# Kernel optimization log

Measured on AMD Instinct MI355X. Metric: run time of the kernel, lower is better.

Reference implementation:

```python
import jax, jax.numpy as jnp
import numpy as np

B, T, HID, H, Dk, Dv, K = 2, 1024, 1024, 8, 128, 128, 4
EPS = 1e-5


def _dwconv_causal(y, w, b):
    # y: [B,T,C], w: [C,1,K], b: [C]; torch Conv1d(padding=K-1) then [:, :, :T] == causal left-pad
    C = y.shape[-1]
    z = jnp.transpose(y, (0, 2, 1))  # [B,C,T]
    z = jax.lax.conv_general_dilated(
        z, w, window_strides=(1,), padding=[(K - 1, 0)],
        feature_group_count=C, dimension_numbers=("NCH", "OIH", "NCH"))
    z = z + b[None, :, None]
    return jnp.transpose(z, (0, 2, 1))


def _forward(x, Wq, Wk, Wv, conv_q_w, conv_q_b, conv_k_w, conv_k_b,
             conv_v_w, conv_v_b, Wa, ba, Wb, bb, Wg, Wo, ln_g, ln_b):
    b_, t_ = x.shape[0], x.shape[1]
    q = jax.nn.silu(_dwconv_causal(x @ Wq, conv_q_w, conv_q_b))
    k = jax.nn.silu(_dwconv_causal(x @ Wk, conv_k_w, conv_k_b))
    v = jax.nn.silu(_dwconv_causal(x @ Wv, conv_v_w, conv_v_b))
    q = q.reshape(b_, t_, H, Dk)
    k = k.reshape(b_, t_, H, Dk) * (Dk ** -0.5)
    v = v.reshape(b_, t_, H, Dv)
    alpha = jax.nn.sigmoid(x @ Wa + ba)  # [B,T,H]
    beta = jax.nn.sigmoid(x @ Wb + bb)   # [B,T,H]

    # time-major for scan
    qt = jnp.transpose(q, (1, 0, 2, 3))  # [T,B,H,Dk]
    kt = jnp.transpose(k, (1, 0, 2, 3))
    vt = jnp.transpose(v, (1, 0, 2, 3))  # [T,B,H,Dv]
    at = jnp.transpose(alpha, (1, 0, 2))  # [T,B,H]
    bt = jnp.transpose(beta, (1, 0, 2))

    def step(S, inp):
        q_t, k_t, v_t, a_t, b_t = inp
        sk = jnp.einsum('bhij,bhj->bhi', S, k_t)          # S @ k
        err = sk - v_t                                     # [B,H,Dv]
        S = a_t[:, :, None, None] * S - b_t[:, :, None, None] * (err[..., None] * k_t[:, :, None, :])
        o_t = jnp.einsum('bhij,bhj->bhi', S, q_t)          # S @ q (post-update)
        return S, o_t

    S0 = jnp.zeros((b_, H, Dv, Dk), x.dtype)
    _, o = jax.lax.scan(step, S0, (qt, kt, vt, at, bt))
    o = jnp.transpose(o, (1, 0, 2, 3))  # [B,T,H,Dv]

    # LayerNorm over Dv
    mu = jnp.mean(o, axis=-1, keepdims=True)
    var = jnp.mean((o - mu) ** 2, axis=-1, keepdims=True)
    o = (o - mu) * jax.lax.rsqrt(var + EPS) * ln_g + ln_b

    g = jax.nn.sigmoid(x @ Wg).reshape(b_, t_, H, Dv)
    o = (o * g).reshape(b_, t_, H * Dv)
    return o @ Wo


def setup_inputs() -> dict:
    key = jax.random.key(0)
    ks = jax.random.split(key, 18)
    s = 0.02

    def n(k, shape, scale=s):
        return jax.random.normal(k, shape, jnp.float32) * scale

    return {
        "x": jax.random.normal(ks[0], (B, T, HID), jnp.float32),
        "Wq": n(ks[1], (HID, H * Dk)),
        "Wk": n(ks[2], (HID, H * Dk)),
        "Wv": n(ks[3], (HID, H * Dv)),
        "conv_q_w": n(ks[4], (H * Dk, 1, K), 0.25),
        "conv_q_b": n(ks[5], (H * Dk,), 0.1),
        "conv_k_w": n(ks[6], (H * Dk, 1, K), 0.25),
        "conv_k_b": n(ks[7], (H * Dk,), 0.1),
        "conv_v_w": n(ks[8], (H * Dv, 1, K), 0.25),
        "conv_v_b": n(ks[9], (H * Dv,), 0.1),
        "Wa": n(ks[10], (HID, H)),
        "ba": n(ks[11], (H,), 0.1),
        "Wb": n(ks[12], (HID, H)),
        "bb": n(ks[13], (H,), 0.1),
        "Wg": n(ks[14], (HID, H * Dv)),
        "Wo": n(ks[15], (H * Dv, HID)),
        "ln_g": jnp.ones((Dv,), jnp.float32),
        "ln_b": jnp.zeros((Dv,), jnp.float32),
    }


def reference(x, Wq, Wk, Wv, conv_q_w, conv_q_b, conv_k_w, conv_k_b,
              conv_v_w, conv_v_b, Wa, ba, Wb, bb, Wg, Wo, ln_g, ln_b):
    return _forward(x, Wq, Wk, Wv, conv_q_w, conv_q_b, conv_k_w, conv_k_b,
                    conv_v_w, conv_v_b, Wa, ba, Wb, bb, Wg, Wo, ln_g, ln_b)
```

## Files before the change

kernel.cpp:

```cpp
#include <hip/hip_runtime.h>

#define TSEQ 1024
#define HID_ 1024
#define NH 8
#define DK 128
#define DV 128
#define ROWS 2048
#define SZf (ROWS * HID_)
#define LCH 64
#define NCK 16
#define KSTR 136
#define ESTR 65

typedef __attribute__((ext_vector_type(8))) short short8;
typedef __attribute__((ext_vector_type(4))) float f32x4;
#define MFMA __builtin_amdgcn_mfma_f32_16x16x32_bf16

__device__ __forceinline__ float sig_(float x) { return 1.f / (1.f + __expf(-x)); }

__device__ __forceinline__ ushort f2bf(float f) {
    unsigned int u = __builtin_bit_cast(unsigned int, f);
    u += 0x7FFF + ((u >> 16) & 1);
    return (ushort)(u >> 16);
}
__device__ __forceinline__ unsigned int pk2(float lo, float hi) {
    return (unsigned int)f2bf(lo) | ((unsigned int)f2bf(hi) << 16);
}

__global__ __launch_bounds__(256)
void k_x2bf(const float* __restrict__ x, ushort* __restrict__ xb)
{
    const size_t i8 = (size_t)blockIdx.x * 256 + threadIdx.x;
    float4 v0 = *(const float4*)(x + i8 * 8);
    float4 v1 = *(const float4*)(x + i8 * 8 + 4);
    uint4 o;
    o.x = pk2(v0.x, v0.y); o.y = pk2(v0.z, v0.w);
    o.z = pk2(v1.x, v1.y); o.w = pk2(v1.z, v1.w);
    *(uint4*)(xb + i8 * 8) = o;
}

__global__ __launch_bounds__(256)
void k_wT(const float* __restrict__ s0, const float* __restrict__ s1,
          const float* __restrict__ s2, const float* __restrict__ s3,
          ushort* __restrict__ dst)
{
    const int z = blockIdx.z;
    const float* W = (z == 0) ? s0 : (z == 1) ? s1 : (z == 2) ? s2 : s3;
    ushort* WT = dst + (size_t)z * (1024 * 1024);
    __shared__ float t[64][65];
    const int n0 = blockIdx.x * 64, k0 = blockIdx.y * 64;
    const int rr = threadIdx.x >> 4, cc = threadIdx.x & 15;
#pragma unroll
    for (int i = 0; i < 4; ++i) {
        const int row = i * 16 + rr;
        float4 v = *(const float4*)(W + (size_t)(k0 + row) * 1024 + n0 + cc * 4);
        t[row][cc * 4 + 0] = v.x; t[row][cc * 4 + 1] = v.y;
// ... 143 lines not shown
void k_conv_apply(float* __restrict__ q, float* __restrict__ k, float* __restrict__ v,
                  const float* __restrict__ scr,
                  const float* __restrict__ wq, const float* __restrict__ bq,
                  const float* __restrict__ wk, const float* __restrict__ bk,
                  const float* __restrict__ wv, const float* __restrict__ bv)
{
    const int z = blockIdx.z, b = blockIdx.y;
    const int j = blockIdx.x >> 2, cg = blockIdx.x & 3;
    float* y          = (z == 0) ? q  : (z == 1) ? k  : v;
    const float* w    = (z == 0) ? wq : (z == 1) ? wk : wv;
    const float* bias = (z == 0) ? bq : (z == 1) ? bk : bv;
    const float scale = (z == 1) ? 0.08838834764831845f : 1.f;
    const int c = cg * 256 + threadIdx.x;
    const float w0 = w[c * 4], w1 = w[c * 4 + 1], w2 = w[c * 4 + 2], w3 = w[c * 4 + 3];
    const float bs = bias[c];
    float y0 = 0.f, y1 = 0.f, y2 = 0.f;
    if (j > 0) {
        const float* s = scr + ((size_t)(z * 2 + b) * 15 + (j - 1)) * 3 * 1024 + c;
        y0 = s[0]; y1 = s[1024]; y2 = s[2048];
    }
    float* yp = y + ((size_t)b * TSEQ + j * 64) * HID_ + c;
#pragma unroll 4
    for (int t = 0; t < 64; ++t) {
        float y3  = yp[(size_t)t * HID_];
        float acc = fmaf(w0, y0, fmaf(w1, y1, fmaf(w2, y2, fmaf(w3, y3, bs))));
        float sv  = acc * sig_(acc) * scale;
        yp[(size_t)t * HID_] = sv;
        y0 = y1; y1 = y2; y2 = y3;
    }
}

__global__ __launch_bounds__(256)
void k_stage(const float* __restrict__ klin, const float* __restrict__ qlin,
             ushort* __restrict__ Kst, ushort* __restrict__ Qst,
             ushort* __restrict__ KTst)
{
    const int cid = blockIdx.x;
    const int bh = cid >> 4, c = cid & 15;
    const int b = bh >> 3, h = bh & 7;
    const int tid = threadIdx.x;
    const int t0 = c * LCH;
    __shared__ ushort Kl[64 * KSTR];
    const float* kb = klin + ((size_t)b * TSEQ + t0) * HID_ + h * DK;
    const float* qb = qlin + ((size_t)b * TSEQ + t0) * HID_ + h * DK;
    const size_t go = (size_t)cid * 8192;
#pragma unroll
    for (int j = 0; j < 8; ++j) {
        const int i4 = tid + j * 256;
        const int row = i4 >> 5, c4 = i4 & 31;
        float4 kv = *(const float4*)(kb + (size_t)row * HID_ + c4 * 4);
        float4 qv = *(const float4*)(qb + (size_t)row * HID_ + c4 * 4);
        uint2 kp; kp.x = pk2(kv.x, kv.y); kp.y = pk2(kv.z, kv.w);
        uint2 qp; qp.x = pk2(qv.x, qv.y); qp.y = pk2(qv.z, qv.w);
        *(uint2*)(Kst + go + row * 128 + c4 * 4) = kp;
        *(uint2*)(Qst + go + row * 128 + c4 * 4) = qp;
        *(uint2*)(Kl + row * KSTR + c4 * 4) = kp;
    }
    __syncthreads();
#pragma unroll
    for (int j = 0; j < 4; ++j) {
        const int o8 = tid + j * 256;
        const int dk = o8 >> 3, tt = (o8 & 7) * 8;
        ushort tmp[8];
#pragma unroll
        for (int e = 0; e < 8; ++e) tmp[e] = Kl[(tt + e) * KSTR + dk];
        *(uint4*)(KTst + go + dk * 64 + tt) = *(uint4*)tmp;
    }
}

__global__ __launch_bounds__(256)
void k_prep(const ushort* __restrict__ Kst, const ushort* __restrict__ Qst,
            const float* __restrict__ aT, const float* __restrict__ bT,
            ushort* __restrict__ Mg, ushort* __restrict__ Gg,
            float* __restrict__ pug, float* __restrict__ pog,
            float* __restrict__ cg, float* __restrict__ dtotg)
{
    const int cid = blockIdx.x;
    const int bh = cid >> 4, c = cid & 15;
    const int tid = threadIdx.x;
    const int t0 = c * LCH;

    __shared__ ushort Kb[64 * KSTR], Qb[64 * KSTR];
    __shared__ float Ef[64 * ESTR];
    __shared__ float Mf[64 * ESTR];
    __shared__ float cums[64], bv[64];

    if (tid < 64) {
        const float a = aT[(size_t)bh * TSEQ + t0 + tid];
        bv[tid] = bT[(size_t)bh * TSEQ + t0 + tid];
        float cs = __logf(a);
#pragma unroll
        for (int d = 1; d < 64; d <<= 1) {
            float pv = __shfl_up(cs, d);
            if (tid >= d) cs += pv;
        }
        cums[tid] = cs;
    }
    const size_t go = (size_t)cid * 8192;
#pragma unroll
// ... 41 lines not shown

    if (tid < 64) {
        const int s = tid;
        for (int r = 0; r < 64; ++r) Mf[r * ESTR + s] = 0.f;
        Mf[s * ESTR + s] = bv[s];
        for (int t = 1; t < 64; ++t) {
            float s0 = 0.f, s1 = 0.f;
            int r = 0;
            for (; r + 1 < t; r += 2) {
                s0 = fmaf(Ef[t * ESTR + r],     Mf[r * ESTR + s],       s0);
                s1 = fmaf(Ef[t * ESTR + r + 1], Mf[(r + 1) * ESTR + s], s1);
            }
            if (r < t) s0 = fmaf(Ef[t * ESTR + r], Mf[r * ESTR + s], s0);
            if (s < t) Mf[t * ESTR + s] = -bv[t] * (s0 + s1);
        }
    }
    __syncthreads();
    ushort* Mc = Mg + (size_t)cid * 4096;
#pragma unroll
    for (int j = 0; j < 16; ++j) {
        const int e = tid + j * 256;
        Mc[e] = f2bf(Mf[(e >> 6) * ESTR + (e & 63)]);
    }
    if (tid < 64) {
        const float cp = (tid > 0) ? cums[tid - 1] : 0.f;
        pug[cid * 64 + tid] = __expf(cp);
        pog[cid * 64 + tid] = __expf(cums[tid]);
        cg [cid * 64 + tid] = __expf(cums[63] - cums[tid]);
        if (tid == 0) dtotg[cid] = __expf(cums[63]);
    }
}

__global__ __launch_bounds__(256)
void k_scan2(const ushort* __restrict__ Kst, const ushort* __restrict__ Qst,
             const ushort* __restrict__ KTst, const float* __restrict__ vlin,
             const ushort* __restrict__ Mg, const ushort* __restrict__ Gg,
             const float* __restrict__ pug, const float* __restrict__ pog,
             const float* __restrict__ cg, const float* __restrict__ dtotg,
             float* __restrict__ o)
{
    const int blk = blockIdx.x;
    const int bh = blk >> 2, rb = blk & 3;
    const int b = bh >> 3, h = bh & 7;
    const int tid = threadIdx.x;
    const int wv = tid >> 6, l = tid & 63, l15 = l & 15, lq = l >> 4;
    const int k8o = lq * 8;

    __shared__ ushort Kb[64 * KSTR], Qb[64 * KSTR];
    __shared__ ushort KTb[128 * 72];
    __shared__ float  Vtf[32 * 72];
    __shared__ ushort Mb[64 * 72], Gb[64 * 72];
    __shared__ ushort Shb[32 * KSTR], Slb[32 * KSTR];
    __shared__ ushort Yb[32 * 72], Wb[32 * 72], Wcb[32 * 72];
    __shared__ float  Otf[64 * 36];
    __shared__ float  puv[64], pov[64], cv2[64], dts[1];

    const int trow  = wv >> 1;
    const int tcol0 = (wv & 1) * 2;
    const int scol0 = (wv & 1) * 4;

    f32x4 accS[4];
#pragma unroll
    for (int m = 0; m < 4; ++m) accS[m] = f32x4{0.f, 0.f, 0.f, 0.f};

    const float* vbase = vlin + (size_t)b * TSEQ * HID_ + h * DV + rb * 32;
    float* obase = o + (size_t)bh * TSEQ * DV + rb * 32;

    uint4 rk[4], rq[4], rkt[4], rm[2], rg[2];
    float4 rv[2];
    float rpu = 0.f, rpo = 0.f, rcv = 0.f, rdt = 0.f;

    auto LOADC = [&](int cc) {
        const int cid = bh * 16 + cc;
        const size_t go = (size_t)cid * 8192;
#pragma unroll
        for (int j = 0; j < 4; ++j) {
            rk[j]  = *(const uint4*)(Kst  + go + (tid + j * 256) * 8);
            rq[j]  = *(const uint4*)(Qst  + go + (tid + j * 256) * 8);
            rkt[j] = *(const uint4*)(KTst + go + (tid + j * 256) * 8);
        }
#pragma unroll
        for (int j = 0; j < 2; ++j) {
            rm[j] = *(const uint4*)(Mg + (size_t)cid * 4096 + (tid + j * 256) * 8);
            rg[j] = *(const uint4*)(Gg + (size_t)cid * 4096 + (tid + j * 256) * 8);
            const int i4 = tid + j * 256;
            rv[j] = *(const float4*)(vbase + (size_t)(cc * LCH + (i4 >> 3)) * HID_ + (i4 & 7) * 4);
        }
        if (tid < 64) {
            rpu = pug[cid * 64 + tid];
            rpo = pog[cid * 64 + tid];
            rcv = cg [cid * 64 + tid];
            if (tid == 0) rdt = dtotg[cid];
        }
    };
    auto WRITEC = [&]() {
#pragma unroll
        for (int j = 0; j < 4; ++j) {
            const int i16 = tid + j * 256;
            *(uint4*)(Kb  + (i16 >> 4) * KSTR + (i16 & 15) * 8) = rk[j];
            *(uint4*)(Qb  + (i16 >> 4) * KSTR + (i16 & 15) * 8) = rq[j];
            *(uint4*)(KTb + (i16 >> 3) * 72   + (i16 & 7) * 8)  = rkt[j];
        }
#pragma unroll
        for (int j = 0; j < 2; ++j) {
            const int i8 = tid + j * 256;
            *(uint4*)(Mb + (i8 >> 3) * 72 + (i8 & 7) * 8) = rm[j];
            *(uint4*)(Gb + (i8 >> 3) * 72 + (i8 & 7) * 8) = rg[j];
            const int i4 = tid + j * 256;
            const int row = i4 >> 3, c4 = i4 & 7;
            Vtf[(c4 * 4 + 0) * 72 + row] = rv[j].x;
            Vtf[(c4 * 4 + 1) * 72 + row] = rv[j].y;
            Vtf[(c4 * 4 + 2) * 72 + row] = rv[j].z;
            Vtf[(c4 * 4 + 3) * 72 + row] = rv[j].w;
        }
        if (tid < 64) {
            puv[tid] = rpu; pov[tid] = rpo; cv2[tid] = rcv;
            if (tid == 0) dts[0] = rdt;
        }
    };

    LOADC(0);
    WRITEC();
    __syncthreads();

    for (int c = 0; c < NCK; ++c) {
        const int t0 = c * LCH;
        if (c + 1 < NCK) LOADC(c + 1);

#pragma unroll
        for (int m = 0; m < 4; ++m) {
#pragma unroll
            for (int r = 0; r < 4; ++r) {
                const int dv = trow * 16 + lq * 4 + r;
                const int dk = (scol0 + m) * 16 + l15;
                const float sv = accS[m][r];
                const ushort hi = f2bf(sv);
                const float hf = __builtin_bit_cast(float, ((unsigned)hi) << 16);
                Shb[dv * KSTR + dk] = hi;
                Slb[dv * KSTR + dk] = f2bf(sv - hf);
            }
        }
        __syncthreads();

        f32x4 accU[2], accQ[2];
#pragma unroll
        for (int jj = 0; jj < 2; ++jj) {
            accU[jj] = f32x4{0.f, 0.f, 0.f, 0.f};
            accQ[jj] = f32x4{0.f, 0.f, 0.f, 0.f};
        }
#pragma unroll
        for (int kk = 0; kk < 4; ++kk) {
            short8 ah = *(const short8*)(Shb + (trow * 16 + l15) * KSTR + kk * 32 + k8o);
            short8 al = *(const short8*)(Slb + (trow * 16 + l15) * KSTR + kk * 32 + k8o);
#pragma unroll
            for (int jj = 0; jj < 2; ++jj) {
                short8 bk = *(const short8*)(Kb + ((tcol0 + jj) * 16 + l15) * KSTR + kk * 32 + k8o);
                short8 bq = *(const short8*)(Qb + ((tcol0 + jj) * 16 + l15) * KSTR + kk * 32 + k8o);
                accU[jj] = MFMA(ah, bk, accU[jj], 0, 0, 0);
                accU[jj] = MFMA(al, bk, accU[jj], 0, 0, 0);
                accQ[jj] = MFMA(ah, bq, accQ[jj], 0, 0, 0);
                accQ[jj] = MFMA(al, bq, accQ[jj], 0, 0, 0);
            }
        }
#pragma unroll
        for (int jj = 0; jj < 2; ++jj) {
#pragma unroll
            for (int r = 0; r < 4; ++r) {
                const int t = (tcol0 + jj) * 16 + l15;
                const int dv = trow * 16 + lq * 4 + r;
                const float y = Vtf[dv * 72 + t] - puv[t] * accU[jj][r];
                Yb[dv * 72 + t] = f2bf(y);
            }
        }
        __syncthreads();

        f32x4 accW[2];
#pragma unroll
        for (int jj = 0; jj < 2; ++jj) accW[jj] = f32x4{0.f, 0.f, 0.f, 0.f};
#pragma unroll
        for (int kk = 0; kk < 2; ++kk) {
            short8 ay = *(const short8*)(Yb + (trow * 16 + l15) * 72 + kk * 32 + k8o);
#pragma unroll
            for (int jj = 0; jj < 2; ++jj) {
                short8 bm = *(const short8*)(Mb + ((tcol0 + jj) * 16 + l15) * 72 + kk * 32 + k8o);
                accW[jj] = MFMA(ay, bm, accW[jj], 0, 0, 0);
            }
        }
#pragma unroll
        for (int jj = 0; jj < 2; ++jj) {
#pragma unroll
            for (int r = 0; r < 4; ++r) {
                const int t = (tcol0 + jj) * 16 + l15;
                const int dv = trow * 16 + lq * 4 + r;
                const float wvl = accW[jj][r];
                Wb[dv * 72 + t]  = f2bf(wvl);
                Wcb[dv * 72 + t] = f2bf(wvl * cv2[t]);
            }
        }
        __syncthreads();

        f32x4 accO[2];
#pragma unroll
        for (int jj = 0; jj < 2; ++jj) accO[jj] = f32x4{0.f, 0.f, 0.f, 0.f};
#pragma unroll
        for (int kk = 0; kk < 2; ++kk) {
            short8 aw = *(const short8*)(Wb + (trow * 16 + l15) * 72 + kk * 32 + k8o);
#pragma unroll
            for (int jj = 0; jj < 2; ++jj) {
                short8 bg = *(const short8*)(Gb + ((tcol0 + jj) * 16 + l15) * 72 + kk * 32 + k8o);
                accO[jj] = MFMA(aw, bg, accO[jj], 0, 0, 0);
            }
        }
#pragma unroll
        for (int jj = 0; jj < 2; ++jj) {
#pragma unroll
            for (int r = 0; r < 4; ++r) {
                const int t = (tcol0 + jj) * 16 + l15;
                const int dv = trow * 16 + lq * 4 + r;
                Otf[t * 36 + dv] = pov[t] * accQ[jj][r] + accO[jj][r];
            }
        }
        const float dt = dts[0];
#pragma unroll
        for (int m = 0; m < 4; ++m)
#pragma unroll
            for (int r = 0; r < 4; ++r) accS[m][r] *= dt;
#pragma unroll
        for (int kk = 0; kk < 2; ++kk) {
            short8 aw = *(const short8*)(Wcb + (trow * 16 + l15) * 72 + kk * 32 + k8o);
#pragma unroll
            for (int m = 0; m < 4; ++m) {
                short8 bk = *(const short8*)(KTb + ((scol0 + m) * 16 + l15) * 72 + kk * 32 + k8o);
                accS[m] = MFMA(aw, bk, accS[m], 0, 0, 0);
            }
        }
        __syncthreads();

#pragma unroll
        for (int j = 0; j < 2; ++j) {
            const int i4 = tid + j * 256;
            const int row = i4 >> 3, c4 = i4 & 7;
            float4 ov = *(const float4*)(Otf + row * 36 + c4 * 4);
            *(float4*)(obase + (size_t)(t0 + row) * DV + c4 * 4) = ov;
        }
        if (c + 1 < NCK) WRITEC();
        __syncthreads();
    }
}

__global__ __launch_bounds__(256)
void k_ln_gate(const float* __restrict__ o, const float* __restrict__ g_lin,
               const float* __restrict__ ln_g, const float* __restrict__ ln_b,
               ushort* __restrict__ ogb)
{
    const int idx  = blockIdx.x * 4 + (threadIdx.x >> 6);
    const int lane = threadIdx.x & 63;
    const int h  = idx & 7;
    const int bt = idx >> 3;
    const int b  = bt >> 10;
    const int t  = bt & 1023;
    const float* op = o + ((size_t)(b * NH + h) * TSEQ + t) * DV;
    float2 xv = ((const float2*)op)[lane];
    float s = xv.x + xv.y;
#pragma unroll
    for (int m = 32; m; m >>= 1) s += __shfl_xor(s, m);
    const float mu = s * (1.f / 128.f);
    const float d0 = xv.x - mu, d1 = xv.y - mu;
    float v = d0 * d0 + d1 * d1;
#pragma unroll
    for (int m = 32; m; m >>= 1) v += __shfl_xor(v, m);
    const float inv = rsqrtf(v * (1.f / 128.f) + 1e-5f);
    const int d = lane * 2;
    const float* gp = g_lin + (size_t)bt * HID_ + h * DV;
    const float g0 = sig_(gp[d]), g1 = sig_(gp[d + 1]);
    const float y0 = (d0 * inv * ln_g[d]     + ln_b[d])     * g0;
    const float y1 = (d1 * inv * ln_g[d + 1] + ln_b[d + 1]) * g1;
    *(uint*)(ogb + (size_t)bt * HID_ + h * DV + d) = pk2(y0, y1);
}

extern "C" void kernel_launch(void* const* d_in, const int* in_sizes, int n_in,
                              void* d_out, int out_size, void* d_ws, size_t ws_size,
                              hipStream_t stream)
{
    const float* x   = (const float*)d_in[0];
    const float* Wq  = (const float*)d_in[1];
    const float* Wk  = (const float*)d_in[2];
    const float* Wv  = (const float*)d_in[3];
    const float* cqw = (const float*)d_in[4];
    const float* cqb = (const float*)d_in[5];
    const float* ckw = (const float*)d_in[6];
    const float* ckb = (const float*)d_in[7];
    const float* cvw = (const float*)d_in[8];
    const float* cvb = (const float*)d_in[9];
    const float* Wa  = (const float*)d_in[10];
    const float* ba  = (const float*)d_in[11];
    const float* Wb  = (const float*)d_in[12];
    const float* bb  = (const float*)d_in[13];
    const float* Wg  = (const float*)d_in[14];
    const float* Wo  = (const float*)d_in[15];
    const float* lng = (const float*)d_in[16];
    const float* lnb = (const float*)d_in[17];
    float* out = (float*)d_out;
    float* ws  = (float*)d_ws;

    float* q_lin = ws;
    float* k_lin = ws + 1 * (size_t)SZf;
    float* v_lin = ws + 2 * (size_t)SZf;
    float* g_lin = ws + 3 * (size_t)SZf;
    float* o_buf = ws + 4 * (size_t)SZf;
    float* aT    = ws + 5 * (size_t)SZf;
    float* bT    = aT + 16 * TSEQ;
    float* pug   = bT + 16 * TSEQ;
    float* pog   = pug + 256 * 64;
    float* cgd   = pog + 256 * 64;
    float* dtg   = cgd + 256 * 64;

    float*  tail = ws + 5 * (size_t)SZf + 131072;
    ushort* Kst  = (ushort*)tail;
    ushort* Qst  = Kst + (size_t)256 * 8192;
    ushort* xbf  = Qst + (size_t)256 * 8192;

    ushort* WT4 = (ushort*)o_buf;
    ushort* WoT = (ushort*)k_lin;
    ushort* ogb = (ushort*)q_lin;
    ushort* Mg  = (ushort*)out;
    ushort* Gg  = Mg + (size_t)256 * 4096;
    ushort* KTst = Gg + (size_t)256 * 4096;

    k_x2bf<<<1024, 256, 0, stream>>>(x, xbf);
    k_wT<<<dim3(16, 16, 4), 256, 0, stream>>>(Wq, Wk, Wv, Wg, WT4);
    k_gemm4<<<dim3(8, 16, 4), 256, 0, stream>>>(xbf, WT4, ws);
    k_ab<<<ROWS, 64, 0, stream>>>(x, Wa, ba, Wb, bb, aT, bT);
    k_conv_save<<<dim3(15, 2, 3), 256, 0, stream>>>(q_lin, k_lin, v_lin, o_buf);
    k_conv_apply<<<dim3(64, 2, 3), 256, 0, stream>>>(q_lin, k_lin, v_lin, o_buf,
                                                     cqw, cqb, ckw, ckb, cvw, cvb);
    k_stage<<<256, 256, 0, stream>>>(k_lin, q_lin, Kst, Qst, KTst);
    k_prep<<<256, 256, 0, stream>>>(Kst, Qst, aT, bT, Mg, Gg, pug, pog, cgd, dtg);
    k_wT<<<dim3(16, 16, 1), 256, 0, stream>>>(Wo, Wo, Wo, Wo, WoT);
    k_scan2<<<64, 256, 0, stream>>>(Kst, Qst, KTst, v_lin, Mg, Gg,
                                    pug, pog, cgd, dtg, o_buf);
    k_ln_gate<<<4096, 256, 0, stream>>>(o_buf, g_lin, lng, lnb, ogb);
    k_gemm1<<<dim3(8, 16), 256, 0, stream>>>(ogb, WoT, out);
}
```

Before: 230.4 us.

## Warp-specialize scan kernel into producer and consumer wavefronts

Splits the 4 wavefronts of the chunked delta-rule scan kernel into two compute waves, each owning 16 dv rows across all t and dk columns, and two producer waves that do the global loads, the shared-memory staging and the output stores. The consumer waves no longer need block barriers between the internal matmul stages, so each chunk step drops from five syncthreads to two. The cost is half the MFMA throughput per block and roughly double the accumulator and staging registers per thread, with the compute chain serialized on two waves.

```diff
diff --git a/kernel.cpp b/kernel.cpp
--- a/kernel.cpp
+++ b/kernel.cpp
@@ -384,6 +384,7 @@
     const int tid = threadIdx.x;
     const int wv = tid >> 6, l = tid & 63, l15 = l & 15, lq = l >> 4;
     const int k8o = lq * 8;
+    const int st = tid - 128;
 
     __shared__ ushort Kb[64 * KSTR], Qb[64 * KSTR];
     __shared__ ushort KTb[128 * 72];
@@ -394,195 +395,189 @@
     __shared__ float  Otf[64 * 36];
     __shared__ float  puv[64], pov[64], cv2[64], dts[1];
 
-    const int trow  = wv >> 1;
-    const int tcol0 = (wv & 1) * 2;
-    const int scol0 = (wv & 1) * 4;
-
-    f32x4 accS[4];
-#pragma unroll
-    for (int m = 0; m < 4; ++m) accS[m] = f32x4{0.f, 0.f, 0.f, 0.f};
+    f32x4 accS[8];
+#pragma unroll
+    for (int m = 0; m < 8; ++m) accS[m] = f32x4{0.f, 0.f, 0.f, 0.f};
 
     const float* vbase = vlin + (size_t)b * TSEQ * HID_ + h * DV + rb * 32;
     float* obase = o + (size_t)bh * TSEQ * DV + rb * 32;
 
-    uint4 rk[4], rq[4], rkt[4], rm[2], rg[2];
-    float4 rv[2];
+    uint4 rk[8], rq[8], rkt[8], rm[4], rg[4];
+    float4 rv[4];
     float rpu = 0.f, rpo = 0.f, rcv = 0.f, rdt = 0.f;
 
     auto LOADC = [&](int cc) {
         const int cid = bh * 16 + cc;
         const size_t go = (size_t)cid * 8192;
 #pragma unroll
+        for (int j = 0; j < 8; ++j) {
+            const int i16 = st + j * 128;
+            rk[j]  = *(const uint4*)(Kst  + go + i16 * 8);
+            rq[j]  = *(const uint4*)(Qst  + go + i16 * 8);
+            rkt[j] = *(const uint4*)(KTst + go + i16 * 8);
+        }
+#pragma unroll
         for (int j = 0; j < 4; ++j) {
-            rk[j]  = *(const uint4*)(Kst  + go + (tid + j * 256) * 8);
-            rq[j]  = *(const uint4*)(Qst  + go + (tid + j * 256) * 8);
-            rkt[j] = *(const uint4*)(KTst + go + (tid + j * 256) * 8);
-        }
-#pragma unroll
-        for (int j = 0; j < 2; ++j) {
-            rm[j] = *(const uint4*)(Mg + (size_t)cid * 4096 + (tid + j * 256) * 8);
-            rg[j] = *(const uint4*)(Gg + (size_t)cid * 4096 + (tid + j * 256) * 8);
-            const int i4 = tid + j * 256;
-            rv[j] = *(const float4*)(vbase + (size_t)(cc * LCH + (i4 >> 3)) * HID_ + (i4 & 7) * 4);
-        }
-        if (tid < 64) {
-            rpu = pug[cid * 64 + tid];
-            rpo = pog[cid * 64 + tid];
-            rcv = cg [cid * 64 + tid];
-            if (tid == 0) rdt = dtotg[cid];
+            const int i8 = st + j * 128;
+            rm[j] = *(const uint4*)(Mg + (size_t)cid * 4096 + i8 * 8);
+            rg[j] = *(const uint4*)(Gg + (size_t)cid * 4096 + i8 * 8);
+            rv[j] = *(const float4*)(vbase + (size_t)(cc * LCH + (i8 >> 3)) * HID_ + (i8 & 7) * 4);
+        }
+        if (st < 64) {
+            rpu = pug[cid * 64 + st];
+            rpo = pog[cid * 64 + st];
+            rcv = cg [cid * 64 + st];
+            if (st == 0) rdt = dtotg[cid];
         }
     };
     auto WRITEC = [&]() {
 #pragma unroll
-        for (int j = 0; j < 4; ++j) {
-            const int i16 = tid + j * 256;
+        for (int j = 0; j < 8; ++j) {
+            const int i16 = st + j * 128;
             *(uint4*)(Kb  + (i16 >> 4) * KSTR + (i16 & 15) * 8) = rk[j];
             *(uint4*)(Qb  + (i16 >> 4) * KSTR + (i16 & 15) * 8) = rq[j];
             *(uint4*)(KTb + (i16 >> 3) * 72   + (i16 & 7) * 8)  = rkt[j];
         }
 #pragma unroll
-        for (int j = 0; j < 2; ++j) {
-            const int i8 = tid + j * 256;
+        for (int j = 0; j < 4; ++j) {
+            const int i8 = st + j * 128;
             *(uint4*)(Mb + (i8 >> 3) * 72 + (i8 & 7) * 8) = rm[j];
             *(uint4*)(Gb + (i8 >> 3) * 72 + (i8 & 7) * 8) = rg[j];
-            const int i4 = tid + j * 256;
-            const int row = i4 >> 3, c4 = i4 & 7;
+            const int row = i8 >> 3, c4 = i8 & 7;
             Vtf[(c4 * 4 + 0) * 72 + row] = rv[j].x;
             Vtf[(c4 * 4 + 1) * 72 + row] = rv[j].y;
             Vtf[(c4 * 4 + 2) * 72 + row] = rv[j].z;
             Vtf[(c4 * 4 + 3) * 72 + row] = rv[j].w;
         }
-        if (tid < 64) {
-            puv[tid] = rpu; pov[tid] = rpo; cv2[tid] = rcv;
-            if (tid == 0) dts[0] = rdt;
+        if (st < 64) {
+            puv[st] = rpu; pov[st] = rpo; cv2[st] = rcv;
+            if (st == 0) dts[0] = rdt;
         }
     };
 
-    LOADC(0);
-    WRITEC();
+    if (wv >= 2) { LOADC(0); WRITEC(); }
     __syncthreads();
 
     for (int c = 0; c < NCK; ++c) {
         const int t0 = c * LCH;
-        if (c + 1 < NCK) LOADC(c + 1);
-
-#pragma unroll
-        for (int m = 0; m < 4; ++m) {
-#pragma unroll
-            for (int r = 0; r < 4; ++r) {
-                const int dv = trow * 16 + lq * 4 + r;
-                const int dk = (scol0 + m) * 16 + l15;
-                const float sv = accS[m][r];
-                const ushort hi = f2bf(sv);
-                const float hf = __builtin_bit_cast(float, ((unsigned)hi) << 16);
-                Shb[dv * KSTR + dk] = hi;
-                Slb[dv * KSTR + dk] = f2bf(sv - hf);
+        if (wv >= 2) {
+            if (c + 1 < NCK) LOADC(c + 1);
+        } else {
+#pragma unroll
+            for (int m = 0; m < 8; ++m) {
+#pragma unroll
+                for (int r = 0; r < 4; ++r) {
+                    const int dv = wv * 16 + lq * 4 + r;
+                    const int dk = m * 16 + l15;
+                    const float sv = accS[m][r];
+                    const ushort hi = f2bf(sv);
+                    const float hf = __builtin_bit_cast(float, ((unsigned)hi) << 16);
+                    Shb[dv * KSTR + dk] = hi;
+                    Slb[dv * KSTR + dk] = f2bf(sv - hf);
+                }
+            }
+            f32x4 accU[4], accQ[4];
+#pragma unroll
+            for (int jj = 0; jj < 4; ++jj) {
+                accU[jj] = f32x4{0.f, 0.f, 0.f, 0.f};
+                accQ[jj] = f32x4{0.f, 0.f, 0.f, 0.f};
+            }
+#pragma unroll
+            for (int kk = 0; kk < 4; ++kk) {
+                short8 ah = *(const short8*)(Shb + (wv * 16 + l15) * KSTR + kk * 32 + k8o);
+                short8 al = *(const short8*)(Slb + (wv * 16 + l15) * KSTR + kk * 32 + k8o);
+#pragma unroll
+                for (int jj = 0; jj < 4; ++jj) {
+                    short8 bk = *(const short8*)(Kb + (jj * 16 + l15) * KSTR + kk * 32 + k8o);
+                    short8 bq = *(const short8*)(Qb + (jj * 16 + l15) * KSTR + kk * 32 + k8o);
+                    accU[jj] = MFMA(ah, bk, accU[jj], 0, 0, 0);
+                    accU[jj] = MFMA(al, bk, accU[jj], 0, 0, 0);
+                    accQ[jj] = MFMA(ah, bq, accQ[jj], 0, 0, 0);
+                    accQ[jj] = MFMA(al, bq, accQ[jj], 0, 0, 0);
+                }
+            }
+#pragma unroll
+            for (int jj = 0; jj < 4; ++jj) {
+                const int t = jj * 16 + l15;
+                const float pu = puv[t];
+#pragma unroll
+                for (int r = 0; r < 4; ++r) {
+                    const int dv = wv * 16 + lq * 4 + r;
+                    Yb[dv * 72 + t] = f2bf(Vtf[dv * 72 + t] - pu * accU[jj][r]);
+                }
+            }
+            f32x4 accW[4];
+#pragma unroll
+            for (int jj = 0; jj < 4; ++jj) accW[jj] = f32x4{0.f, 0.f, 0.f, 0.f};
+#pragma unroll
+            for (int kk = 0; kk < 2; ++kk) {
+                short8 ay = *(const short8*)(Yb + (wv * 16 + l15) * 72 + kk * 32 + k8o);
+#pragma unroll
+                for (int jj = 0; jj < 4; ++jj) {
+                    short8 bm = *(const short8*)(Mb + (jj * 16 + l15) * 72 + kk * 32 + k8o);
+                    accW[jj] = MFMA(ay, bm, accW[jj], 0, 0, 0);
+                }
+            }
+#pragma unroll
+            for (int jj = 0; jj < 4; ++jj) {
+                const int t = jj * 16 + l15;
+                const float cvt = cv2[t];
+#pragma unroll
+                for (int r = 0; r < 4; ++r) {
+                    const int dv = wv * 16 + lq * 4 + r;
+                    const float wvl = accW[jj][r];
+                    Wb[dv * 72 + t]  = f2bf(wvl);
+                    Wcb[dv * 72 + t] = f2bf(wvl * cvt);
+                }
+            }
+            f32x4 accO[4];
+#pragma unroll
+            for (int jj = 0; jj < 4; ++jj) accO[jj] = f32x4{0.f, 0.f, 0.f, 0.f};
+#pragma unroll
+            for (int kk = 0; kk < 2; ++kk) {
+                short8 aw = *(const short8*)(Wb + (wv * 16 + l15) * 72 + kk * 32 + k8o);
+#pragma unroll
+                for (int jj = 0; jj < 4; ++jj) {
+                    short8 bg = *(const short8*)(Gb + (jj * 16 + l15) * 72 + kk * 32 + k8o);
+                    accO[jj] = MFMA(aw, bg, accO[jj], 0, 0, 0);
+                }
+            }
+#pragma unroll
+            for (int jj = 0; jj < 4; ++jj) {
+                const int t = jj * 16 + l15;
+                const float po = pov[t];
+#pragma unroll
+                for (int r = 0; r < 4; ++r) {
+                    const int dv = wv * 16 + lq * 4 + r;
+                    Otf[t * 36 + dv] = po * accQ[jj][r] + accO[jj][r];
+                }
+            }
+            const float dt = dts[0];
+#pragma unroll
+            for (int m = 0; m < 8; ++m)
+#pragma unroll
+                for (int r = 0; r < 4; ++r) accS[m][r] *= dt;
+#pragma unroll
+            for (int kk = 0; kk < 2; ++kk) {
+                short8 aw = *(const short8*)(Wcb + (wv * 16 + l15) * 72 + kk * 32 + k8o);
+#pragma unroll
+                for (int m = 0; m < 8; ++m) {
+                    short8 bk = *(const short8*)(KTb + (m * 16 + l15) * 72 + kk * 32 + k8o);
+                    accS[m] = MFMA(aw, bk, accS[m], 0, 0, 0);
+                }
             }
         }
         __syncthreads();
-
-        f32x4 accU[2], accQ[2];
-#pragma unroll
-        for (int jj = 0; jj < 2; ++jj) {
-            accU[jj] = f32x4{0.f, 0.f, 0.f, 0.f};
-            accQ[jj] = f32x4{0.f, 0.f, 0.f, 0.f};
-        }
-#pragma unroll
-        for (int kk = 0; kk < 4; ++kk) {
-            short8 ah = *(const short8*)(Shb + (trow * 16 + l15) * KSTR + kk * 32 + k8o);
-            short8 al = *(const short8*)(Slb + (trow * 16 + l15) * KSTR + kk * 32 + k8o);
-#pragma unroll
-            for (int jj = 0; jj < 2; ++jj) {
-                short8 bk = *(const short8*)(Kb + ((tcol0 + jj) * 16 + l15) * KSTR + kk * 32 + k8o);
-                short8 bq = *(const short8*)(Qb + ((tcol0 + jj) * 16 + l15) * KSTR + kk * 32 + k8o);
-                accU[jj] = MFMA(ah, bk, accU[jj], 0, 0, 0);
-                accU[jj] = MFMA(al, bk, accU[jj], 0, 0, 0);
-                accQ[jj] = MFMA(ah, bq, accQ[jj], 0, 0, 0);
-                accQ[jj] = MFMA(al, bq, accQ[jj], 0, 0, 0);
-            }
-        }
-#pragma unroll
-        for (int jj = 0; jj < 2; ++jj) {
-#pragma unroll
-            for (int r = 0; r < 4; ++r) {
-                const int t = (tcol0 + jj) * 16 + l15;
-                const int dv = trow * 16 + lq * 4 + r;
-                const float y = Vtf[dv * 72 + t] - puv[t] * accU[jj][r];
-                Yb[dv * 72 + t] = f2bf(y);
-            }
-        }
-        __syncthreads();
-
-        f32x4 accW[2];
-#pragma unroll
-        for (int jj = 0; jj < 2; ++jj) accW[jj] = f32x4{0.f, 0.f, 0.f, 0.f};
-#pragma unroll
-        for (int kk = 0; kk < 2; ++kk) {
-            short8 ay = *(const short8*)(Yb + (trow * 16 + l15) * 72 + kk * 32 + k8o);
-#pragma unroll
-            for (int jj = 0; jj < 2; ++jj) {
-                short8 bm = *(const short8*)(Mb + ((tcol0 + jj) * 16 + l15) * 72 + kk * 32 + k8o);
-                accW[jj] = MFMA(ay, bm, accW[jj], 0, 0, 0);
-            }
-        }
-#pragma unroll
-        for (int jj = 0; jj < 2; ++jj) {
-#pragma unroll
-            for (int r = 0; r < 4; ++r) {
-                const int t = (tcol0 + jj) * 16 + l15;
-                const int dv = trow * 16 + lq * 4 + r;
-                const float wvl = accW[jj][r];
-                Wb[dv * 72 + t]  = f2bf(wvl);
-                Wcb[dv * 72 + t] = f2bf(wvl * cv2[t]);
-            }
-        }
-        __syncthreads();
-
-        f32x4 accO[2];
-#pragma unroll
-        for (int jj = 0; jj < 2; ++jj) accO[jj] = f32x4{0.f, 0.f, 0.f, 0.f};
-#pragma unroll
-        for (int kk = 0; kk < 2; ++kk) {
-            short8 aw = *(const short8*)(Wb + (trow * 16 + l15) * 72 + kk * 32 + k8o);
-#pragma unroll
-            for (int jj = 0; jj < 2; ++jj) {
-                short8 bg = *(const short8*)(Gb + ((tcol0 + jj) * 16 + l15) * 72 + kk * 32 + k8o);
-                accO[jj] = MFMA(aw, bg, accO[jj], 0, 0, 0);
-            }
-        }
-#pragma unroll
-        for (int jj = 0; jj < 2; ++jj) {
-#pragma unroll
-            for (int r = 0; r < 4; ++r) {
-                const int t = (tcol0 + jj) * 16 + l15;
-                const int dv = trow * 16 + lq * 4 + r;
-                Otf[t * 36 + dv] = pov[t] * accQ[jj][r] + accO[jj][r];
-            }
-        }
-        const float dt = dts[0];
-#pragma unroll
-        for (int m = 0; m < 4; ++m)
-#pragma unroll
-            for (int r = 0; r < 4; ++r) accS[m][r] *= dt;
-#pragma unroll
-        for (int kk = 0; kk < 2; ++kk) {
-            short8 aw = *(const short8*)(Wcb + (trow * 16 + l15) * 72 + kk * 32 + k8o);
-#pragma unroll
-            for (int m = 0; m < 4; ++m) {
-                short8 bk = *(const short8*)(KTb + ((scol0 + m) * 16 + l15) * 72 + kk * 32 + k8o);
-                accS[m] = MFMA(aw, bk, accS[m], 0, 0, 0);
-            }
-        }
-        __syncthreads();
-
-#pragma unroll
-        for (int j = 0; j < 2; ++j) {
-            const int i4 = tid + j * 256;
-            const int row = i4 >> 3, c4 = i4 & 7;
-            float4 ov = *(const float4*)(Otf + row * 36 + c4 * 4);
-            *(float4*)(obase + (size_t)(t0 + row) * DV + c4 * 4) = ov;
-        }
-        if (c + 1 < NCK) WRITEC();
+        if (wv >= 2) {
+#pragma unroll
+            for (int j = 0; j < 4; ++j) {
+                const int i4 = st + j * 128;
+                const int row = i4 >> 3, c4 = i4 & 7;
+                float4 ov = *(const float4*)(Otf + row * 36 + c4 * 4);
+                *(float4*)(obase + (size_t)(t0 + row) * DV + c4 * 4) = ov;
+            }
+            if (c + 1 < NCK) WRITEC();
+        }
         __syncthreads();
     }
 }
```

Result: slower. 335.6 us (+45.7%).

## Move chunk output computation out of the sequential scan into a parallel kernel

Applied to the files above, without the earlier changes.

The sequential state scan (64 blocks) no longer computes per-chunk outputs. It writes each chunk's starting state and W matrix to global memory in bf16, and a new 256-block kernel then computes the intra/inter-chunk outputs with MFMA and fuses them with LayerNorm and gating. V is pre-converted to bf16 and transposed in the staging kernel, and the K transpose is done in shared memory inside the scan. The aim is to shorten the latency-bound serial critical path and drop the separate LN kernel, at the cost of extra global traffic for the per-chunk states.

```diff
diff --git a/kernel.cpp b/kernel.cpp
--- a/kernel.cpp
+++ b/kernel.cpp
@@ -22,6 +22,9 @@
     unsigned int u = __builtin_bit_cast(unsigned int, f);
     u += 0x7FFF + ((u >> 16) & 1);
     return (ushort)(u >> 16);
+}
+__device__ __forceinline__ float bf2f(ushort u) {
+    return __builtin_bit_cast(float, ((unsigned int)u) << 16);
 }
 __device__ __forceinline__ unsigned int pk2(float lo, float hi) {
     return (unsigned int)f2bf(lo) | ((unsigned int)f2bf(hi) << 16);
@@ -231,17 +234,19 @@
 
 __global__ __launch_bounds__(256)
 void k_stage(const float* __restrict__ klin, const float* __restrict__ qlin,
+             const float* __restrict__ vlin,
              ushort* __restrict__ Kst, ushort* __restrict__ Qst,
-             ushort* __restrict__ KTst)
+             ushort* __restrict__ Vst)
 {
     const int cid = blockIdx.x;
     const int bh = cid >> 4, c = cid & 15;
     const int b = bh >> 3, h = bh & 7;
     const int tid = threadIdx.x;
     const int t0 = c * LCH;
-    __shared__ ushort Kl[64 * KSTR];
+    __shared__ ushort Vl[128 * 72];
     const float* kb = klin + ((size_t)b * TSEQ + t0) * HID_ + h * DK;
     const float* qb = qlin + ((size_t)b * TSEQ + t0) * HID_ + h * DK;
+    const float* vb = vlin + ((size_t)b * TSEQ + t0) * HID_ + h * DV;
     const size_t go = (size_t)cid * 8192;
 #pragma unroll
     for (int j = 0; j < 8; ++j) {
@@ -249,21 +254,23 @@
         const int row = i4 >> 5, c4 = i4 & 31;
         float4 kv = *(const float4*)(kb + (size_t)row * HID_ + c4 * 4);
         float4 qv = *(const float4*)(qb + (size_t)row * HID_ + c4 * 4);
+        float4 vv = *(const float4*)(vb + (size_t)row * HID_ + c4 * 4);
         uint2 kp; kp.x = pk2(kv.x, kv.y); kp.y = pk2(kv.z, kv.w);
         uint2 qp; qp.x = pk2(qv.x, qv.y); qp.y = pk2(qv.z, qv.w);
         *(uint2*)(Kst + go + row * 128 + c4 * 4) = kp;
         *(uint2*)(Qst + go + row * 128 + c4 * 4) = qp;
-        *(uint2*)(Kl + row * KSTR + c4 * 4) = kp;
+        const int dv0 = c4 * 4;
+        Vl[(dv0 + 0) * 72 + row] = f2bf(vv.x);
+        Vl[(dv0 + 1) * 72 + row] = f2bf(vv.y);
+        Vl[(dv0 + 2) * 72 + row] = f2bf(vv.z);
+        Vl[(dv0 + 3) * 72 + row] = f2bf(vv.w);
     }
     __syncthreads();
 #pragma unroll
     for (int j = 0; j < 4; ++j) {
-        const int o8 = tid + j * 256;
-        const int dk = o8 >> 3, tt = (o8 & 7) * 8;
-        ushort tmp[8];
-#pragma unroll
-        for (int e = 0; e < 8; ++e) tmp[e] = Kl[(tt + e) * KSTR + dk];
-        *(uint4*)(KTst + go + dk * 64 + tt) = *(uint4*)tmp;
+        const int idx = tid + j * 256;
+        const int dv = idx >> 3, tq = (idx & 7) * 8;
+        *(uint4*)(Vst + go + dv * 64 + tq) = *(const uint4*)(Vl + dv * 72 + tq);
     }
 }
 
@@ -371,101 +378,87 @@
 }
 
 __global__ __launch_bounds__(256)
-void k_scan2(const ushort* __restrict__ Kst, const ushort* __restrict__ Qst,
-             const ushort* __restrict__ KTst, const float* __restrict__ vlin,
-             const ushort* __restrict__ Mg, const ushort* __restrict__ Gg,
-             const float* __restrict__ pug, const float* __restrict__ pog,
-             const float* __restrict__ cg, const float* __restrict__ dtotg,
-             float* __restrict__ o)
+void k_scan2(const ushort* __restrict__ Kst, const ushort* __restrict__ Vst,
+             const ushort* __restrict__ Mg,
+             const float* __restrict__ pug, const float* __restrict__ cgd,
+             const float* __restrict__ dtg,
+             ushort* __restrict__ Sst, ushort* __restrict__ Wst)
 {
     const int blk = blockIdx.x;
     const int bh = blk >> 2, rb = blk & 3;
-    const int b = bh >> 3, h = bh & 7;
     const int tid = threadIdx.x;
     const int wv = tid >> 6, l = tid & 63, l15 = l & 15, lq = l >> 4;
     const int k8o = lq * 8;
-
-    __shared__ ushort Kb[64 * KSTR], Qb[64 * KSTR];
-    __shared__ ushort KTb[128 * 72];
-    __shared__ float  Vtf[32 * 72];
-    __shared__ ushort Mb[64 * 72], Gb[64 * 72];
-    __shared__ ushort Shb[32 * KSTR], Slb[32 * KSTR];
-    __shared__ ushort Yb[32 * 72], Wb[32 * 72], Wcb[32 * 72];
-    __shared__ float  Otf[64 * 36];
-    __shared__ float  puv[64], pov[64], cv2[64], dts[1];
-
     const int trow  = wv >> 1;
     const int tcol0 = (wv & 1) * 2;
     const int scol0 = (wv & 1) * 4;
 
+    __shared__ ushort Kb[64 * KSTR];
+    __shared__ ushort KTb[128 * 72];
+    __shared__ ushort Mb[64 * 72];
+    __shared__ ushort Vb[32 * 72];
+    __shared__ ushort Shb[32 * KSTR], Slb[32 * KSTR];
+    __shared__ ushort Yb[32 * 72], Wb[32 * 72], Wcb[32 * 72];
+    __shared__ float  puv[64], cv2[64], dts[1];
+
     f32x4 accS[4];
 #pragma unroll
     for (int m = 0; m < 4; ++m) accS[m] = f32x4{0.f, 0.f, 0.f, 0.f};
 
-    const float* vbase = vlin + (size_t)b * TSEQ * HID_ + h * DV + rb * 32;
-    float* obase = o + (size_t)bh * TSEQ * DV + rb * 32;
-
-    uint4 rk[4], rq[4], rkt[4], rm[2], rg[2];
-    float4 rv[2];
-    float rpu = 0.f, rpo = 0.f, rcv = 0.f, rdt = 0.f;
+    uint4 rk[4], rm[2], rv;
+    float rpu = 0.f, rcv = 0.f, rdt = 0.f;
 
     auto LOADC = [&](int cc) {
         const int cid = bh * 16 + cc;
         const size_t go = (size_t)cid * 8192;
 #pragma unroll
-        for (int j = 0; j < 4; ++j) {
-            rk[j]  = *(const uint4*)(Kst  + go + (tid + j * 256) * 8);
-            rq[j]  = *(const uint4*)(Qst  + go + (tid + j * 256) * 8);
-            rkt[j] = *(const uint4*)(KTst + go + (tid + j * 256) * 8);
-        }
-#pragma unroll
-        for (int j = 0; j < 2; ++j) {
+        for (int j = 0; j < 4; ++j)
+            rk[j] = *(const uint4*)(Kst + go + (tid + j * 256) * 8);
+#pragma unroll
+        for (int j = 0; j < 2; ++j)
             rm[j] = *(const uint4*)(Mg + (size_t)cid * 4096 + (tid + j * 256) * 8);
-            rg[j] = *(const uint4*)(Gg + (size_t)cid * 4096 + (tid + j * 256) * 8);
-            const int i4 = tid + j * 256;
-            rv[j] = *(const float4*)(vbase + (size_t)(cc * LCH + (i4 >> 3)) * HID_ + (i4 & 7) * 4);
-        }
+        rv = *(const uint4*)(Vst + go + rb * 2048 + tid * 8);
         if (tid < 64) {
             rpu = pug[cid * 64 + tid];
-            rpo = pog[cid * 64 + tid];
-            rcv = cg [cid * 64 + tid];
-            if (tid == 0) rdt = dtotg[cid];
+            rcv = cgd[cid * 64 + tid];
+            if (tid == 0) rdt = dtg[cid];
         }
     };
     auto WRITEC = [&]() {
 #pragma unroll
         for (int j = 0; j < 4; ++j) {
             const int i16 = tid + j * 256;
-            *(uint4*)(Kb  + (i16 >> 4) * KSTR + (i16 & 15) * 8) = rk[j];
-            *(uint4*)(Qb  + (i16 >> 4) * KSTR + (i16 & 15) * 8) = rq[j];
-            *(uint4*)(KTb + (i16 >> 3) * 72   + (i16 & 7) * 8)  = rkt[j];
+            *(uint4*)(Kb + (i16 >> 4) * KSTR + (i16 & 15) * 8) = rk[j];
         }
 #pragma unroll
         for (int j = 0; j < 2; ++j) {
             const int i8 = tid + j * 256;
             *(uint4*)(Mb + (i8 >> 3) * 72 + (i8 & 7) * 8) = rm[j];
-            *(uint4*)(Gb + (i8 >> 3) * 72 + (i8 & 7) * 8) = rg[j];
-            const int i4 = tid + j * 256;
-            const int row = i4 >> 3, c4 = i4 & 7;
-            Vtf[(c4 * 4 + 0) * 72 + row] = rv[j].x;
-            Vtf[(c4 * 4 + 1) * 72 + row] = rv[j].y;
-            Vtf[(c4 * 4 + 2) * 72 + row] = rv[j].z;
-            Vtf[(c4 * 4 + 3) * 72 + row] = rv[j].w;
-        }
+        }
+        *(uint4*)(Vb + (tid >> 3) * 72 + (tid & 7) * 8) = rv;
         if (tid < 64) {
-            puv[tid] = rpu; pov[tid] = rpo; cv2[tid] = rcv;
+            puv[tid] = rpu; cv2[tid] = rcv;
             if (tid == 0) dts[0] = rdt;
         }
     };
 
-    LOADC(0);
-    WRITEC();
+    LOADC(0); WRITEC();
     __syncthreads();
 
     for (int c = 0; c < NCK; ++c) {
-        const int t0 = c * LCH;
         if (c + 1 < NCK) LOADC(c + 1);
-
+#pragma unroll
+        for (int j = 0; j < 4; ++j) {
+            const int i16 = tid + j * 256;
+            const int t = i16 >> 4, dk0 = (i16 & 15) * 8;
+            uint4 v = *(const uint4*)(Kb + t * KSTR + dk0);
+            ushort tmp[8]; *(uint4*)tmp = v;
+#pragma unroll
+            for (int e = 0; e < 8; ++e) {
+                const int ep = (e + (l & 7)) & 7;
+                KTb[(dk0 + ep) * 72 + t] = tmp[ep];
+            }
+        }
 #pragma unroll
         for (int m = 0; m < 4; ++m) {
 #pragma unroll
@@ -480,13 +473,10 @@
             }
         }
         __syncthreads();
-
-        f32x4 accU[2], accQ[2];
-#pragma unroll
-        for (int jj = 0; jj < 2; ++jj) {
-            accU[jj] = f32x4{0.f, 0.f, 0.f, 0.f};
-            accQ[jj] = f32x4{0.f, 0.f, 0.f, 0.f};
-        }
+        const float dt = dts[0];
+        f32x4 accU[2];
+#pragma unroll
+        for (int jj = 0; jj < 2; ++jj) accU[jj] = f32x4{0.f, 0.f, 0.f, 0.f};
 #pragma unroll
         for (int kk = 0; kk < 4; ++kk) {
             short8 ah = *(const short8*)(Shb + (trow * 16 + l15) * KSTR + kk * 32 + k8o);
@@ -494,25 +484,22 @@
 #pragma unroll
             for (int jj = 0; jj < 2; ++jj) {
                 short8 bk = *(const short8*)(Kb + ((tcol0 + jj) * 16 + l15) * KSTR + kk * 32 + k8o);
-                short8 bq = *(const short8*)(Qb + ((tcol0 + jj) * 16 + l15) * KSTR + kk * 32 + k8o);
                 accU[jj] = MFMA(ah, bk, accU[jj], 0, 0, 0);
                 accU[jj] = MFMA(al, bk, accU[jj], 0, 0, 0);
-                accQ[jj] = MFMA(ah, bq, accQ[jj], 0, 0, 0);
-                accQ[jj] = MFMA(al, bq, accQ[jj], 0, 0, 0);
             }
         }
 #pragma unroll
         for (int jj = 0; jj < 2; ++jj) {
+            const int t = (tcol0 + jj) * 16 + l15;
+            const float pu = puv[t];
 #pragma unroll
             for (int r = 0; r < 4; ++r) {
-                const int t = (tcol0 + jj) * 16 + l15;
                 const int dv = trow * 16 + lq * 4 + r;
-                const float y = Vtf[dv * 72 + t] - puv[t] * accU[jj][r];
-                Yb[dv * 72 + t] = f2bf(y);
+                const float vf = bf2f(Vb[dv * 72 + t]);
+                Yb[dv * 72 + t] = f2bf(vf - pu * accU[jj][r]);
             }
         }
         __syncthreads();
-
         f32x4 accW[2];
 #pragma unroll
         for (int jj = 0; jj < 2; ++jj) accW[jj] = f32x4{0.f, 0.f, 0.f, 0.f};
@@ -527,39 +514,17 @@
         }
 #pragma unroll
         for (int jj = 0; jj < 2; ++jj) {
+            const int t = (tcol0 + jj) * 16 + l15;
+            const float cvt = cv2[t];
 #pragma unroll
             for (int r = 0; r < 4; ++r) {
-                const int t = (tcol0 + jj) * 16 + l15;
                 const int dv = trow * 16 + lq * 4 + r;
                 const float wvl = accW[jj][r];
                 Wb[dv * 72 + t]  = f2bf(wvl);
-                Wcb[dv * 72 + t] = f2bf(wvl * cv2[t]);
+                Wcb[dv * 72 + t] = f2bf(wvl * cvt);
             }
         }
         __syncthreads();
-
-        f32x4 accO[2];
-#pragma unroll
-        for (int jj = 0; jj < 2; ++jj) accO[jj] = f32x4{0.f, 0.f, 0.f, 0.f};
-#pragma unroll
-        for (int kk = 0; kk < 2; ++kk) {
-            short8 aw = *(const short8*)(Wb + (trow * 16 + l15) * 72 + kk * 32 + k8o);
-#pragma unroll
-            for (int jj = 0; jj < 2; ++jj) {
-                short8 bg = *(const short8*)(Gb + ((tcol0 + jj) * 16 + l15) * 72 + kk * 32 + k8o);
-                accO[jj] = MFMA(aw, bg, accO[jj], 0, 0, 0);
-            }
-        }
-#pragma unroll
-        for (int jj = 0; jj < 2; ++jj) {
-#pragma unroll
-            for (int r = 0; r < 4; ++r) {
-                const int t = (tcol0 + jj) * 16 + l15;
-                const int dv = trow * 16 + lq * 4 + r;
-                Otf[t * 36 + dv] = pov[t] * accQ[jj][r] + accO[jj][r];
-            }
-        }
-        const float dt = dts[0];
 #pragma unroll
         for (int m = 0; m < 4; ++m)
 #pragma unroll
@@ -573,14 +538,18 @@
                 accS[m] = MFMA(aw, bk, accS[m], 0, 0, 0);
             }
         }
-        __syncthreads();
-
-#pragma unroll
-        for (int j = 0; j < 2; ++j) {
-            const int i4 = tid + j * 256;
-            const int row = i4 >> 3, c4 = i4 & 7;
-            float4 ov = *(const float4*)(Otf + row * 36 + c4 * 4);
-            *(float4*)(obase + (size_t)(t0 + row) * DV + c4 * 4) = ov;
+        {
+            const int cid = bh * 16 + c;
+            const size_t so = (size_t)cid * 16384 + rb * 4096;
+#pragma unroll
+            for (int j = 0; j < 2; ++j) {
+                const int idx = tid + j * 256;
+                const int dvl = idx >> 4, ko = (idx & 15) * 8;
+                *(uint4*)(Sst + so + dvl * 128 + ko) =
+                    *(const uint4*)(Shb + dvl * KSTR + ko);
+            }
+            *(uint4*)(Wst + (size_t)cid * 8192 + rb * 2048 + (tid >> 3) * 64 + (tid & 7) * 8)
+                = *(const uint4*)(Wb + (tid >> 3) * 72 + (tid & 7) * 8);
         }
         if (c + 1 < NCK) WRITEC();
         __syncthreads();
@@ -588,33 +557,115 @@
 }
 
 __global__ __launch_bounds__(256)
-void k_ln_gate(const float* __restrict__ o, const float* __restrict__ g_lin,
-               const float* __restrict__ ln_g, const float* __restrict__ ln_b,
-               ushort* __restrict__ ogb)
-{
-    const int idx  = blockIdx.x * 4 + (threadIdx.x >> 6);
-    const int lane = threadIdx.x & 63;
-    const int h  = idx & 7;
-    const int bt = idx >> 3;
-    const int b  = bt >> 10;
-    const int t  = bt & 1023;
-    const float* op = o + ((size_t)(b * NH + h) * TSEQ + t) * DV;
-    float2 xv = ((const float2*)op)[lane];
-    float s = xv.x + xv.y;
-#pragma unroll
-    for (int m = 32; m; m >>= 1) s += __shfl_xor(s, m);
-    const float mu = s * (1.f / 128.f);
-    const float d0 = xv.x - mu, d1 = xv.y - mu;
-    float v = d0 * d0 + d1 * d1;
-#pragma unroll
-    for (int m = 32; m; m >>= 1) v += __shfl_xor(v, m);
-    const float inv = rsqrtf(v * (1.f / 128.f) + 1e-5f);
-    const int d = lane * 2;
-    const float* gp = g_lin + (size_t)bt * HID_ + h * DV;
-    const float g0 = sig_(gp[d]), g1 = sig_(gp[d + 1]);
-    const float y0 = (d0 * inv * ln_g[d]     + ln_b[d])     * g0;
-    const float y1 = (d1 * inv * ln_g[d + 1] + ln_b[d + 1]) * g1;
-    *(uint*)(ogb + (size_t)bt * HID_ + h * DV + d) = pk2(y0, y1);
+void k_out(const ushort* __restrict__ Sst, const ushort* __restrict__ Qst,
+           const ushort* __restrict__ Gg, const ushort* __restrict__ Wst,
+           const float* __restrict__ pog, const float* __restrict__ g_lin,
+           const float* __restrict__ lng, const float* __restrict__ lnb,
+           ushort* __restrict__ ogb)
+{
+    const int cid = blockIdx.x;
+    const int bh = cid >> 4, c = cid & 15;
+    const int b = bh >> 3, h = bh & 7;
+    const int t0 = c * LCH;
+    const int tid = threadIdx.x;
+    const int wv = tid >> 6, l = tid & 63, l15 = l & 15, lq = l >> 4;
+    const int k8o = lq * 8;
+
+    __shared__ ushort Sb[128 * KSTR];
+    __shared__ ushort Qb[64 * KSTR];
+    __shared__ ushort Gb[64 * 72];
+    __shared__ ushort Wqb[128 * 72];
+    __shared__ float  Ot[64 * 132];
+    __shared__ float  pov[64];
+
+#pragma unroll
+    for (int j = 0; j < 8; ++j) {
+        const int i16 = tid + j * 256;
+        *(uint4*)(Sb + (i16 >> 4) * KSTR + (i16 & 15) * 8) =
+            *(const uint4*)(Sst + (size_t)cid * 16384 + i16 * 8);
+    }
+#pragma unroll
+    for (int j = 0; j < 4; ++j) {
+        const int i16 = tid + j * 256;
+        *(uint4*)(Qb + (i16 >> 4) * KSTR + (i16 & 15) * 8) =
+            *(const uint4*)(Qst + (size_t)cid * 8192 + i16 * 8);
+        const int i8 = i16;
+        *(uint4*)(Wqb + (i8 >> 3) * 72 + (i8 & 7) * 8) =
+            *(const uint4*)(Wst + (size_t)cid * 8192 + i8 * 8);
+    }
+#pragma unroll
+    for (int j = 0; j < 2; ++j) {
+        const int i8 = tid + j * 256;
+        *(uint4*)(Gb + (i8 >> 3) * 72 + (i8 & 7) * 8) =
+            *(const uint4*)(Gg + (size_t)cid * 4096 + i8 * 8);
+    }
+    if (tid < 64) pov[tid] = pog[cid * 64 + tid];
+    __syncthreads();
+
+#pragma unroll
+    for (int i = 0; i < 2; ++i) {
+        const int dvt = wv * 2 + i;
+        f32x4 acc[4], acg[4];
+#pragma unroll
+        for (int jj = 0; jj < 4; ++jj) {
+            acc[jj] = f32x4{0.f, 0.f, 0.f, 0.f};
+            acg[jj] = f32x4{0.f, 0.f, 0.f, 0.f};
+        }
+#pragma unroll
+        for (int kk = 0; kk < 4; ++kk) {
+            short8 sa = *(const short8*)(Sb + (dvt * 16 + l15) * KSTR + kk * 32 + k8o);
+#pragma unroll
+            for (int jj = 0; jj < 4; ++jj) {
+                short8 qb = *(const short8*)(Qb + (jj * 16 + l15) * KSTR + kk * 32 + k8o);
+                acc[jj] = MFMA(sa, qb, acc[jj], 0, 0, 0);
+            }
+        }
+#pragma unroll
+        for (int kk = 0; kk < 2; ++kk) {
+            short8 wa = *(const short8*)(Wqb + (dvt * 16 + l15) * 72 + kk * 32 + k8o);
+#pragma unroll
+            for (int jj = 0; jj < 4; ++jj) {
+                short8 gb = *(const short8*)(Gb + (jj * 16 + l15) * 72 + kk * 32 + k8o);
+                acg[jj] = MFMA(wa, gb, acg[jj], 0, 0, 0);
+            }
+        }
+#pragma unroll
+        for (int jj = 0; jj < 4; ++jj) {
+            const int t = jj * 16 + l15;
+            const float po = pov[t];
+            float4 o4;
+            o4.x = po * acc[jj][0] + acg[jj][0];
+            o4.y = po * acc[jj][1] + acg[jj][1];
+            o4.z = po * acc[jj][2] + acg[jj][2];
+            o4.w = po * acc[jj][3] + acg[jj][3];
+            *(float4*)(Ot + t * 132 + dvt * 16 + lq * 4) = o4;
+        }
+    }
+    __syncthreads();
+
+    const int d = l * 2;
+    const float lg0 = lng[d], lg1 = lng[d + 1];
+    const float lb0 = lnb[d], lb1 = lnb[d + 1];
+    const size_t btbase = (size_t)b * TSEQ + t0 + wv * 16;
+#pragma unroll 1
+    for (int rr = 0; rr < 16; ++rr) {
+        const int t = wv * 16 + rr;
+        float2 xv = *(const float2*)(Ot + t * 132 + d);
+        float s = xv.x + xv.y;
+#pragma unroll
+        for (int m = 32; m; m >>= 1) s += __shfl_xor(s, m);
+        const float mu = s * (1.f / 128.f);
+        const float d0 = xv.x - mu, d1 = xv.y - mu;
+        float v = d0 * d0 + d1 * d1;
+#pragma unroll
+        for (int m = 32; m; m >>= 1) v += __shfl_xor(v, m);
+        const float inv = rsqrtf(v * (1.f / 128.f) + 1e-5f);
+        const float* gp = g_lin + (btbase + rr) * HID_ + h * DV;
+        const float g0 = sig_(gp[d]), g1 = sig_(gp[d + 1]);
+        const float y0 = (d0 * inv * lg0 + lb0) * g0;
+        const float y1 = (d1 * inv * lg1 + lb1) * g1;
+        *(uint*)(ogb + (btbase + rr) * HID_ + h * DV + d) = pk2(y0, y1);
+    }
 }
 
 extern "C" void kernel_launch(void* const* d_in, const int* in_sizes, int n_in,
@@ -658,13 +709,15 @@
     ushort* Kst  = (ushort*)tail;
     ushort* Qst  = Kst + (size_t)256 * 8192;
     ushort* xbf  = Qst + (size_t)256 * 8192;
+    ushort* Vst  = xbf;
 
     ushort* WT4 = (ushort*)o_buf;
     ushort* WoT = (ushort*)k_lin;
     ushort* ogb = (ushort*)q_lin;
+    ushort* Sst = (ushort*)o_buf;
     ushort* Mg  = (ushort*)out;
     ushort* Gg  = Mg + (size_t)256 * 4096;
-    ushort* KTst = Gg + (size_t)256 * 4096;
+    ushort* Wst = Gg + (size_t)256 * 4096;
 
     k_x2bf<<<1024, 256, 0, stream>>>(x, xbf);
     k_wT<<<dim3(16, 16, 4), 256, 0, stream>>>(Wq, Wk, Wv, Wg, WT4);
@@ -673,11 +726,10 @@
     k_conv_save<<<dim3(15, 2, 3), 256, 0, stream>>>(q_lin, k_lin, v_lin, o_buf);
     k_conv_apply<<<dim3(64, 2, 3), 256, 0, stream>>>(q_lin, k_lin, v_lin, o_buf,
                                                      cqw, cqb, ckw, ckb, cvw, cvb);
-    k_stage<<<256, 256, 0, stream>>>(k_lin, q_lin, Kst, Qst, KTst);
+    k_stage<<<256, 256, 0, stream>>>(k_lin, q_lin, v_lin, Kst, Qst, Vst);
     k_prep<<<256, 256, 0, stream>>>(Kst, Qst, aT, bT, Mg, Gg, pug, pog, cgd, dtg);
     k_wT<<<dim3(16, 16, 1), 256, 0, stream>>>(Wo, Wo, Wo, Wo, WoT);
-    k_scan2<<<64, 256, 0, stream>>>(Kst, Qst, KTst, v_lin, Mg, Gg,
-                                    pug, pog, cgd, dtg, o_buf);
-    k_ln_gate<<<4096, 256, 0, stream>>>(o_buf, g_lin, lng, lnb, ogb);
+    k_scan2<<<64, 256, 0, stream>>>(Kst, Vst, Mg, pug, cgd, dtg, Sst, Wst);
+    k_out<<<256, 256, 0, stream>>>(Sst, Qst, Gg, Wst, pog, g_lin, lng, lnb, ogb);
     k_gemm1<<<dim3(8, 16), 256, 0, stream>>>(ogb, WoT, out);
 }
```

New measurement: 237.1 us. +2.9%, slower.
